# Kernel tuning notes

Measured on AMD Instinct MI355X. Metric: run time of the kernel, lower is better.

Reference implementation:

```python
import jax, jax.numpy as jnp
import numpy as np

N_NODES = 100000
N_EDGES = 3200000
N_GRAPHS = 512
IN_CH = 128
HID = 32
OUT = 2


def setup_inputs() -> dict:
    key = jax.random.key(0)
    ks = jax.random.split(key, 6)
    x = jax.random.normal(ks[0], (N_NODES, IN_CH), dtype=jnp.float32)
    edge_index = jax.random.randint(ks[1], (2, N_EDGES), 0, N_NODES, dtype=jnp.int64)
    batch = jnp.sort(jax.random.randint(ks[2], (N_NODES,), 0, N_GRAPHS, dtype=jnp.int64))
    # Glorot-ish params
    W1 = jax.random.normal(ks[3], (IN_CH, HID), dtype=jnp.float32) * (1.0 / np.sqrt(IN_CH))
    b1 = jnp.zeros((HID,), dtype=jnp.float32)
    W2 = jax.random.normal(ks[4], (HID, HID), dtype=jnp.float32) * (1.0 / np.sqrt(HID))
    b2 = jnp.zeros((HID,), dtype=jnp.float32)
    Wl = jax.random.normal(ks[5], (HID, OUT), dtype=jnp.float32) * (1.0 / np.sqrt(HID))
    bl = jnp.zeros((OUT,), dtype=jnp.float32)
    return {"x": x, "edge_index": edge_index, "batch": batch,
            "W1": W1, "b1": b1, "W2": W2, "b2": b2, "Wl": Wl, "bl": bl}


def _gcn_conv(h, src, dst, W, b, n_nodes):
    # PyG GCNConv: transform, add self-loops, symmetric deg normalization,
    # scatter-add messages from src -> dst, then bias.
    h = h @ W  # [N, F_out]
    ones = jnp.ones(src.shape[0], dtype=h.dtype)
    # degree on target nodes, +1 for the implicit self-loop
    deg = jax.ops.segment_sum(ones, dst, num_segments=n_nodes) + 1.0
    dinv = jax.lax.rsqrt(deg)  # deg >= 1 always
    norm = dinv[src] * dinv[dst]  # [E]
    agg = jax.ops.segment_sum(h[src] * norm[:, None], dst, num_segments=n_nodes)
    # self-loop contribution: norm_ii = dinv_i^2
    agg = agg + h * (dinv * dinv)[:, None]
    return agg + b


def reference(x, edge_index, batch, W1, b1, W2, b2, Wl, bl):
    n_nodes = x.shape[0]
    src, dst = edge_index[0], edge_index[1]
    h = jax.nn.relu(_gcn_conv(x, src, dst, W1, b1, n_nodes))
    h = jax.nn.relu(_gcn_conv(h, src, dst, W2, b2, n_nodes))
    # global mean pool per graph
    sums = jax.ops.segment_sum(h, batch, num_segments=N_GRAPHS)
    counts = jax.ops.segment_sum(jnp.ones(n_nodes, h.dtype), batch, num_segments=N_GRAPHS)
    pooled = sums / jnp.maximum(counts, 1.0)[:, None]  # [G, 32]
    return pooled @ Wl + bl  # [G, 2]
```

## Files before the change

kernel.cpp:

```cpp
#include <hip/hip_runtime.h>
#include <hip/hip_bf16.h>

#define N_NODES 100000
#define N_EDGES 3200000
#define N_GRAPHS 512
#define NBUK 782
#define CAP 4608
#define CCAP 5632
#define FILL_CHUNK 8192
#define FILL_BLOCKS ((N_EDGES + FILL_CHUNK - 1) / FILL_CHUNK)
#define GEMM1_BLOCKS ((N_NODES + 63) / 64)

__device__ __forceinline__ float blo(unsigned v) { return __uint_as_float(v << 16); }
__device__ __forceinline__ float bhi(unsigned v) { return __uint_as_float(v & 0xffff0000u); }

__global__ __launch_bounds__(1024) void k_fatA(const int* __restrict__ ei,
                                               int* __restrict__ gcnt,
                                               unsigned* __restrict__ packed,
                                               const float* __restrict__ x,
                                               const float* __restrict__ W1,
                                               float* __restrict__ H1u) {
    __shared__ __align__(16) char smem[49152];
    int t = threadIdx.x;
    if (blockIdx.x < FILL_BLOCKS) {
        unsigned* buf = (unsigned*)smem;
        int* h    = (int*)(smem + 32768);
        int* base = (int*)(smem + 35896);
        int* sb   = (int*)(smem + 39024);
        int* ws   = (int*)(smem + 42152);
        for (int i = t; i < NBUK; i += 1024) h[i] = 0;
        __syncthreads();
        int s0 = blockIdx.x * FILL_CHUNK;
        int ng = min(FILL_CHUNK, N_EDGES - s0) >> 2;
        const int4* src4 = (const int4*)(ei + s0);
        const int4* dst4 = (const int4*)(ei + N_EDGES + s0);
        int4 sv[2], dv[2];
        int  rk[2][4];
#pragma unroll
        for (int g = 0; g < 2; g++) {
            int gi = t + g * 1024;
            if (gi < ng) {
                sv[g] = src4[gi];
                dv[g] = dst4[gi];
                rk[g][0] = atomicAdd(&h[dv[g].x >> 7], 1);
                rk[g][1] = atomicAdd(&h[dv[g].y >> 7], 1);
                rk[g][2] = atomicAdd(&h[dv[g].z >> 7], 1);
                rk[g][3] = atomicAdd(&h[dv[g].w >> 7], 1);
            }
        }
        __syncthreads();
        for (int i = t; i < NBUK; i += 1024) {
            int c = h[i];
            base[i] = c ? atomicAdd(&gcnt[i], c) : 0;
        }
        int lane = t & 63, wv = t >> 6;
        int hval = (t < NBUK) ? h[t] : 0;
        int v = hval;
#pragma unroll
        for (int d2 = 1; d2 < 64; d2 <<= 1) {
            int o = __shfl_up(v, d2);
            if (lane >= d2) v += o;
        }
        if (lane == 63) ws[wv] = v;
        __syncthreads();
        if (wv == 0) {
            int s = (lane < 16) ? ws[lane] : 0;
            int sv2 = s;
#pragma unroll
            for (int d2 = 1; d2 < 16; d2 <<= 1) {
                int o = __shfl_up(sv2, d2);
                if (lane >= d2) sv2 += o;
            }
            if (lane < 16) ws[lane] = sv2 - s;
        }
        __syncthreads();
        if (t < NBUK) sb[t] = v + ws[wv] - hval;
        __syncthreads();
#pragma unroll
        for (int g = 0; g < 2; g++) {
            int gi = t + g * 1024;
            if (gi < ng) {
                int s[4] = {sv[g].x, sv[g].y, sv[g].z, sv[g].w};
                int d[4] = {dv[g].x, dv[g].y, dv[g].z, dv[g].w};
#pragma unroll
                for (int k = 0; k < 4; k++) {
                    int bk = d[k] >> 7;
                    buf[sb[bk] + rk[g][k]] = (unsigned)s[k] | (((unsigned)d[k] & 127u) << 17);
                }
            }
        }
        __syncthreads();
        int w = t >> 6;
        for (int bk = w; bk < NBUK; bk += 16) {
            int c = h[bk];
            if (!c) continue;
            unsigned* gp = packed + (size_t)bk * CAP + base[bk];
            int lb = sb[bk];
            for (int j = lane; j < c; j += 64) gp[j] = buf[lb + j];
        }
    } else {
        float* Ws = (float*)smem;
        float* xs = (float*)(smem + 16384);
        int b = blockIdx.x - FILL_BLOCKS;
        ((float4*)Ws)[t] = ((const float4*)W1)[t];
        int row0 = b * 64;
        const float4* x4 = (const float4*)(x + (size_t)row0 * 128);
        float4* xs4 = (float4*)xs;
        int maxr = min(64, N_NODES - row0);
        int nf4 = maxr * 32;
#pragma unroll
        for (int i = 0; i < 8; i++) {
            int idx = t + i * 1024;
            if (idx < nf4) xs4[idx] = x4[idx];
        }
        __syncthreads();
        int col = t & 31;
        int g = t >> 5;
        int r0 = 2 * g, r1 = 2 * g + 1;
        const float4* xa4 = xs4 + r0 * 32;
        const float4* xb4 = xs4 + r1 * 32;
        float a0 = 0.f, a1 = 0.f;
#pragma unroll 8
        for (int k4 = 0; k4 < 32; k4++) {
            float4 xa = xa4[k4];
            float4 xb = xb4[k4];
            float w0 = Ws[(k4 * 4 + 0) * 32 + col];
            float w1 = Ws[(k4 * 4 + 1) * 32 + col];
            float w2 = Ws[(k4 * 4 + 2) * 32 + col];
            float w3 = Ws[(k4 * 4 + 3) * 32 + col];
            a0 += xa.x * w0 + xa.y * w1 + xa.z * w2 + xa.w * w3;
            a1 += xb.x * w0 + xb.y * w1 + xb.z * w2 + xb.w * w3;
        }
        if (row0 + r0 < N_NODES) H1u[(size_t)(row0 + r0) * 32 + col] = a0;
        if (row0 + r1 < N_NODES) H1u[(size_t)(row0 + r1) * 32 + col] = a1;
    }
}

__global__ __launch_bounds__(512) void k_csr(const unsigned* __restrict__ packed,
                                             const int* __restrict__ gcnt,
                                             int* __restrict__ rp, int* __restrict__ rpe,
                                             float* __restrict__ dinv,
                                             int* __restrict__ csr,
                                             const float* __restrict__ H1u,
                                             __hip_bfloat16* __restrict__ H1s) {
    __shared__ int deg[128];
    __shared__ int nb0[128];
    __shared__ float dsh[128];
    __shared__ int wsum0;
    __shared__ int ntot;
    __shared__ int lcsr[CCAP] __attribute__((aligned(16)));
    int t = threadIdx.x;
    int b = blockIdx.x;
    if (t < 128) deg[t] = 0;
    __syncthreads();
    int n = gcnt[b];
    const unsigned* pb = packed + (size_t)b * CAP;
    unsigned pv[3][4];
    int rk[3][4];
#pragma unroll
    for (int g = 0; g < 3; g++) {
        int i0 = 4 * (t + g * 512);
        if (i0 < n) {
            if (i0 + 3 < n) {
                uint4 p = *(const uint4*)(pb + i0);
                pv[g][0] = p.x; pv[g][1] = p.y; pv[g][2] = p.z; pv[g][3] = p.w;
            } else {
#pragma unroll
                for (int k = 0; k < 4; k++) pv[g][k] = (i0 + k < n) ? pb[i0 + k] : 0u;
            }
#pragma unroll
            for (int k = 0; k < 4; k++)
                if (i0 + k < n) rk[g][k] = atomicAdd(&deg[pv[g][k] >> 17], 1);
        }
    }
    __syncthreads();
    int lane = t & 63;
    int d = (t < 128) ? deg[t] : 0;
    int p16 = (d + 15) & ~15;
    int v = (t < 128) ? p16 : 0;
#pragma unroll
    for (int d2 = 1; d2 < 64; d2 <<= 1) {
        int o = __shfl_up(v, d2);
        if (lane >= d2) v += o;
    }
    if (t == 63) wsum0 = v;
    __syncthreads();
    if (t < 128) {
        int inc = v + ((t >= 64) ? wsum0 : 0);
        int l0 = inc - p16;
        nb0[t] = l0;
        float di = rsqrtf((float)d + 1.0f);
        dsh[t] = di;
        int node = b * 128 + t;
        if (node < N_NODES) {
            rp[node] = b * CCAP + l0;
            rpe[node] = b * CCAP + l0 + p16;
            dinv[node] = di;
        }
        for (int j = d; j < p16; j++) lcsr[l0 + j] = N_NODES;
        if (t == 127) ntot = l0 + p16;
    }
    __syncthreads();
#pragma unroll
    for (int g = 0; g < 3; g++) {
        int i0 = 4 * (t + g * 512);
        if (i0 < n) {
#pragma unroll
            for (int k = 0; k < 4; k++) {
                if (i0 + k < n) {
                    unsigned p = pv[g][k];
                    lcsr[nb0[p >> 17] + rk[g][k]] = (int)(p & 0x1FFFFu);
                }
            }
        }
    }
    __syncthreads();
    int nq = (ntot + 3) >> 2;
    int4* dst4 = (int4*)(csr + (size_t)b * CCAP);
    const int4* sl4 = (const int4*)lcsr;
    for (int i = t; i < nq; i += 512) dst4[i] = sl4[i];
    for (int i = t; i < 1024; i += 512) {
        int row = i >> 3, q = i & 7;
        int node = b * 128 + row;
        if (node < N_NODES) {
            float4 fv = ((const float4*)H1u)[(size_t)node * 8 + q];
            float di = dsh[row];
            __hip_bfloat16 tmp[4];
            tmp[0] = __float2bfloat16(fv.x * di);
            tmp[1] = __float2bfloat16(fv.y * di);
            tmp[2] = __float2bfloat16(fv.z * di);
            tmp[3] = __float2bfloat16(fv.w * di);
            *(uint2*)(H1s + (size_t)node * 32 + q * 4) = *(uint2*)tmp;
        }
    }
    if (b == 0 && t < 16) ((unsigned*)(H1s + (size_t)N_NODES * 32))[t] = 0u;
}

__global__ void k_gather(const __hip_bfloat16* __restrict__ Hs, const float* __restrict__ dinv,
                         const int* __restrict__ rp, const int* __restrict__ rpe,
                         const int* __restrict__ csr,
                         const float* __restrict__ bias, float* __restrict__ hout) {
    int lane = threadIdx.x & 63;
    int fb = lane & 3;
    int qn = lane >> 4;
    int wave = (blockIdx.x * 256 + threadIdx.x) >> 6;
    int wid = wave * 4 + qn;
    const uint4* H4 = (const uint4*)Hs;
    int beg = rp[wid];
    int pdeg = rpe[wid] - beg;
    int sidx = (lane & 48) | ((lane >> 2) & 3);
    float a0=0.f,a1=0.f,a2=0.f,a3=0.f,a4=0.f,a5=0.f,a6=0.f,a7=0.f;
    for (int eb = 0; eb < pdeg; eb += 16) {
        int cv = csr[beg + eb + (lane & 15)];
#pragma unroll
        for (int k = 0; k < 4; k++) {
            int src = __shfl(cv, sidx + 4 * k);
            uint4 v = H4[(unsigned)src * 4u + fb];
            a0 += blo(v.x); a1 += bhi(v.x);
            a2 += blo(v.y); a3 += bhi(v.y);
            a4 += blo(v.z); a5 += bhi(v.z);
            a6 += blo(v.w); a7 += bhi(v.w);
        }
    }
#pragma unroll
    for (int m = 4; m <= 8; m <<= 1) {
        a0 += __shfl_xor(a0, m); a1 += __shfl_xor(a1, m);
        a2 += __shfl_xor(a2, m); a3 += __shfl_xor(a3, m);
        a4 += __shfl_xor(a4, m); a5 += __shfl_xor(a5, m);
        a6 += __shfl_xor(a6, m); a7 += __shfl_xor(a7, m);
    }
    if (((lane >> 2) & 3) == 0) {
        float di = dinv[wid];
        uint4 vw = H4[(unsigned)wid * 4u + fb];
        float4 bA = *(const float4*)(bias + fb * 8);
        float4 bB = *(const float4*)(bias + fb * 8 + 4);
        float4 oA, oB;
        oA.x = fmaxf((a0 + blo(vw.x)) * di + bA.x, 0.f);
        oA.y = fmaxf((a1 + bhi(vw.x)) * di + bA.y, 0.f);
        oA.z = fmaxf((a2 + blo(vw.y)) * di + bA.z, 0.f);
        oA.w = fmaxf((a3 + bhi(vw.y)) * di + bA.w, 0.f);
        oB.x = fmaxf((a4 + blo(vw.z)) * di + bB.x, 0.f);
        oB.y = fmaxf((a5 + bhi(vw.z)) * di + bB.y, 0.f);
        oB.z = fmaxf((a6 + blo(vw.w)) * di + bB.z, 0.f);
        oB.w = fmaxf((a7 + bhi(vw.w)) * di + bB.w, 0.f);
        float* o = hout + (size_t)wid * 32 + fb * 8;
        *(float4*)o = oA;
        *(float4*)(o + 4) = oB;
    }
}

__global__ void k_gemm2(const float* __restrict__ h1, const float* __restrict__ W2,
                        const float* __restrict__ dinv, __hip_bfloat16* __restrict__ H2s) {
    __shared__ float Ws[32 * 32];
    __shared__ float xs[32 * 32];
    int t = threadIdx.x;
    ((float4*)Ws)[t] = ((const float4*)W2)[t];
    int row0 = blockIdx.x * 32;
    ((float4*)xs)[t] = ((const float4*)(h1 + (size_t)row0 * 32))[t];
    __syncthreads();
    int col = t & 31;
    int rb = (t >> 5) * 4;
    float a0 = 0.f, a1 = 0.f, a2 = 0.f, a3 = 0.f;
#pragma unroll
    for (int k = 0; k < 32; k++) {
        float w = Ws[k * 32 + col];
        a0 += xs[(rb + 0) * 32 + k] * w;
        a1 += xs[(rb + 1) * 32 + k] * w;
        a2 += xs[(rb + 2) * 32 + k] * w;
        a3 += xs[(rb + 3) * 32 + k] * w;
    }
    int r = row0 + rb;
    __hip_bfloat16* o = H2s + (size_t)r * 32 + col;
    o[0]  = __float2bfloat16(a0 * dinv[r + 0]);
    o[32] = __float2bfloat16(a1 * dinv[r + 1]);
    o[64] = __float2bfloat16(a2 * dinv[r + 2]);
    o[96] = __float2bfloat16(a3 * dinv[r + 3]);
    if (blockIdx.x == 0 && t < 16) ((unsigned*)(H2s + (size_t)N_NODES * 32))[t] = 0u;
}

__global__ __launch_bounds__(256) void k_pool(const float* __restrict__ h2,
                                              const int* __restrict__ batch,
                                              const float* __restrict__ Wl,
                                              const float* __restrict__ bl,
                                              float* __restrict__ out) {
    __shared__ float red[256];
    __shared__ float pooled[32];
    int g = blockIdx.x;
    int t = threadIdx.x;
    int lo = 0, hi = N_NODES;
    while (lo < hi) { int m = (lo + hi) >> 1; if (batch[m] < g) lo = m + 1; else hi = m; }
    int s = lo;
    hi = N_NODES;
    while (lo < hi) { int m = (lo + hi) >> 1; if (batch[m] < g + 1) lo = m + 1; else hi = m; }
    int e = lo;
    int f = t & 31, r0 = t >> 5;
    float acc = 0.f;
    for (int r = s + r0; r < e; r += 8) acc += h2[(size_t)r * 32 + f];
    red[t] = acc;
    __syncthreads();
    for (int off = 128; off >= 32; off >>= 1) {
        if (t < off) red[t] += red[t + off];
        __syncthreads();
    }
    if (t < 32) pooled[t] = red[t] / fmaxf((float)(e - s), 1.0f);
    __syncthreads();
    if (t < 2) {
        float a = bl[t];
#pragma unroll
        for (int k = 0; k < 32; k++) a += pooled[k] * Wl[k * 2 + t];
        out[g * 2 + t] = a;
    }
}

extern "C" void kernel_launch(void* const* d_in, const int* in_sizes, int n_in,
                              void* d_out, int out_size, void* d_ws, size_t ws_size,
                              hipStream_t stream) {
    const float* x    = (const float*)d_in[0];
    const int*   ei   = (const int*)d_in[1];
    const int*   batch= (const int*)d_in[2];
    const float* W1   = (const float*)d_in[3];
    const float* b1   = (const float*)d_in[4];
    const float* W2   = (const float*)d_in[5];
    const float* b2   = (const float*)d_in[6];
    const float* Wl   = (const float*)d_in[7];
    const float* bl   = (const float*)d_in[8];
    float* out = (float*)d_out;

    char* w = (char*)d_ws;
    size_t off = 0;
    auto take = [&](size_t bytes) -> char* {
        char* p = w + off;
        off = (off + bytes + 255) & ~(size_t)255;
        return p;
    };
    __hip_bfloat16* H1s = (__hip_bfloat16*)take((size_t)(N_NODES + 1) * 32 * 2);
    float*          h1  = (float*)take((size_t)N_NODES * 32 * 4);
    char*           shared = take((size_t)NBUK * CAP * 4);
    unsigned*       packed = (unsigned*)shared;
    __hip_bfloat16* H2s    = (__hip_bfloat16*)shared;
    int*      csr    = (int*)  take((size_t)NBUK * CCAP * 4 + 1024);
    float*    dinv   = (float*)take((size_t)N_NODES * 4);
    int*      rp     = (int*)  take((size_t)N_NODES * 4);
    int*      rpe    = (int*)  take((size_t)N_NODES * 4);
    int*      gcnt   = (int*)  take((size_t)NBUK * 4);

    hipMemsetAsync(gcnt, 0, (size_t)NBUK * 4, stream);

    k_fatA  <<<FILL_BLOCKS + GEMM1_BLOCKS, 1024, 0, stream>>>(ei, gcnt, packed, x, W1, h1);
    k_csr   <<<NBUK, 512, 0, stream>>>(packed, gcnt, rp, rpe, dinv, csr, h1, H1s);
    k_gather<<<N_NODES / 16, 256, 0, stream>>>(H1s, dinv, rp, rpe, csr, b1, h1);
    k_gemm2 <<<N_NODES / 32, 256, 0, stream>>>(h1, W2, dinv, H2s);
    k_gather<<<N_NODES / 16, 256, 0, stream>>>(H2s, dinv, rp, rpe, csr, b2, h1);
    k_pool  <<<N_GRAPHS, 256, 0, stream>>>(h1, batch, Wl, bl, out);
}
```

Measured before the change: 255.0 us.

## Privatize degree counters, use 16-lane bucket copies, unroll gather by 32 edges

The bucket copy-out in the fill kernel now gives each bucket to a 16-thread group instead of a 64-thread wave, which suits the small per-bucket counts. The CSR kernel splits the shared degree histogram into four copies indexed by thread quarter, which cuts LDS atomic contention, and recombines them with prefix offsets. The gather kernel loads two CSR entries per lane and processes 32 edges per iteration, with a 16-edge tail, to keep more loads in flight. The cost is extra index arithmetic and somewhat higher register pressure.

```diff
diff --git a/kernel.cpp b/kernel.cpp
--- a/kernel.cpp
+++ b/kernel.cpp
@@ -90,13 +90,14 @@
             }
         }
         __syncthreads();
-        int w = t >> 6;
-        for (int bk = w; bk < NBUK; bk += 16) {
+        int g16 = t >> 4;
+        int l16 = t & 15;
+        for (int bk = g16; bk < NBUK; bk += 64) {
             int c = h[bk];
             if (!c) continue;
             unsigned* gp = packed + (size_t)bk * CAP + base[bk];
             int lb = sb[bk];
-            for (int j = lane; j < c; j += 64) gp[j] = buf[lb + j];
+            for (int j = l16; j < c; j += 16) gp[j] = buf[lb + j];
         }
     } else {
         float* Ws = (float*)smem;
@@ -143,7 +144,7 @@
                                              int* __restrict__ csr,
                                              const float* __restrict__ H1u,
                                              __hip_bfloat16* __restrict__ H1s) {
-    __shared__ int deg[128];
+    __shared__ int deg4[4][128];
     __shared__ int nb0[128];
     __shared__ float dsh[128];
     __shared__ int wsum0;
@@ -151,10 +152,11 @@
     __shared__ int lcsr[CCAP] __attribute__((aligned(16)));
     int t = threadIdx.x;
     int b = blockIdx.x;
-    if (t < 128) deg[t] = 0;
+    deg4[t >> 7][t & 127] = 0;
     __syncthreads();
     int n = gcnt[b];
     const unsigned* pb = packed + (size_t)b * CAP;
+    int cp = t >> 7;
     unsigned pv[3][4];
     int rk[3][4];
 #pragma unroll
@@ -170,12 +172,16 @@
             }
 #pragma unroll
             for (int k = 0; k < 4; k++)
-                if (i0 + k < n) rk[g][k] = atomicAdd(&deg[pv[g][k] >> 17], 1);
+                if (i0 + k < n) rk[g][k] = atomicAdd(&deg4[cp][pv[g][k] >> 17], 1);
         }
     }
     __syncthreads();
     int lane = t & 63;
-    int d = (t < 128) ? deg[t] : 0;
+    int d = 0, e1 = 0, e2 = 0, e3 = 0;
+    if (t < 128) {
+        int c0 = deg4[0][t], c1 = deg4[1][t], c2 = deg4[2][t], c3 = deg4[3][t];
+        e1 = c0; e2 = c0 + c1; e3 = e2 + c2; d = e3 + c3;
+    }
     int p16 = (d + 15) & ~15;
     int v = (t < 128) ? p16 : 0;
 #pragma unroll
@@ -186,6 +192,7 @@
     if (t == 63) wsum0 = v;
     __syncthreads();
     if (t < 128) {
+        deg4[0][t] = 0; deg4[1][t] = e1; deg4[2][t] = e2; deg4[3][t] = e3;
         int inc = v + ((t >= 64) ? wsum0 : 0);
         int l0 = inc - p16;
         nb0[t] = l0;
@@ -209,7 +216,8 @@
             for (int k = 0; k < 4; k++) {
                 if (i0 + k < n) {
                     unsigned p = pv[g][k];
-                    lcsr[nb0[p >> 17] + rk[g][k]] = (int)(p & 0x1FFFFu);
+                    int dst = p >> 17;
+                    lcsr[nb0[dst] + deg4[cp][dst] + rk[g][k]] = (int)(p & 0x1FFFFu);
                 }
             }
         }
@@ -248,13 +256,16 @@
     const uint4* H4 = (const uint4*)Hs;
     int beg = rp[wid];
     int pdeg = rpe[wid] - beg;
-    int sidx = (lane & 48) | ((lane >> 2) & 3);
+    int grp = lane & 48;
+    int es = (lane >> 2) & 3;
+    int es4 = es * 4;
     float a0=0.f,a1=0.f,a2=0.f,a3=0.f,a4=0.f,a5=0.f,a6=0.f,a7=0.f;
-    for (int eb = 0; eb < pdeg; eb += 16) {
-        int cv = csr[beg + eb + (lane & 15)];
-#pragma unroll
-        for (int k = 0; k < 4; k++) {
-            int src = __shfl(cv, sidx + 4 * k);
+    int e = 0;
+    for (; e + 32 <= pdeg; e += 32) {
+        int2 cv2 = *(const int2*)(csr + beg + e + 2 * (lane & 15));
+#pragma unroll
+        for (int k = 0; k < 8; k++) {
+            int src = __shfl((k & 1) ? cv2.y : cv2.x, grp | (es4 + (k >> 1)));
             uint4 v = H4[(unsigned)src * 4u + fb];
             a0 += blo(v.x); a1 += bhi(v.x);
             a2 += blo(v.y); a3 += bhi(v.y);
@@ -262,6 +273,18 @@
             a6 += blo(v.w); a7 += bhi(v.w);
         }
     }
+    if (e < pdeg) {
+        int cv = csr[beg + e + (lane & 15)];
+#pragma unroll
+        for (int k = 0; k < 4; k++) {
+            int src = __shfl(cv, grp | (es + 4 * k));
+            uint4 v = H4[(unsigned)src * 4u + fb];
+            a0 += blo(v.x); a1 += bhi(v.x);
+            a2 += blo(v.y); a3 += bhi(v.y);
+            a4 += blo(v.z); a5 += bhi(v.z);
+            a6 += blo(v.w); a7 += bhi(v.w);
+        }
+    }
 #pragma unroll
     for (int m = 4; m <= 8; m <<= 1) {
         a0 += __shfl_xor(a0, m); a1 += __shfl_xor(a1, m);
@@ -269,7 +292,7 @@
         a4 += __shfl_xor(a4, m); a5 += __shfl_xor(a5, m);
         a6 += __shfl_xor(a6, m); a7 += __shfl_xor(a7, m);
     }
-    if (((lane >> 2) & 3) == 0) {
+    if (es == 0) {
         float di = dinv[wid];
         uint4 vw = H4[(unsigned)wid * 4u + fb];
         float4 bA = *(const float4*)(bias + fb * 8);
```

Measured after the change: 248.3 us. -2.6%, faster.
